# Performance work log

Measured on AMD Instinct MI355X. Metric: run time of the kernel, lower is better.

Reference implementation:

```python
import jax, jax.numpy as jnp
import numpy as np

N, E, H, NH, S, EF, K = 25000, 400000, 64, 4, 16, 8, 2
HS = H // NH  # head size


def _ln(x, w, b):
    m = x.mean(-1, keepdims=True)
    v = ((x - m) ** 2).mean(-1, keepdims=True)
    return (x - m) / jnp.sqrt(v + 1e-5) * w + b


def _seg_softmax(scores, seg, n):
    # scores: [E, NH], seg: [E] -> softmax over edges sharing the same dest node
    mx = jax.ops.segment_max(scores, seg, num_segments=n)
    e = jnp.exp(scores - mx[seg])
    s = jax.ops.segment_sum(e, seg, num_segments=n)
    return e / (s[seg] + 1e-9)


def _edge_layer(h, x_s, src, dest, ef, w1, w2, proj, gated):
    # h: [N,H] (already layer-normed). Gather, fused per-edge MLP (no bias).
    inp = jnp.concatenate([h[src], h[dest], x_s[src], x_s[dest], ef], axis=-1)  # [E,168]
    raw = jnp.maximum(inp @ w1.T, 0.0) @ w2.T  # [E,NH]
    if gated:
        w = jax.nn.sigmoid(raw)
    else:
        w = _seg_softmax(jax.nn.leaky_relu(raw) / jnp.sqrt(jnp.asarray(HS, raw.dtype)), dest, N)
    msg = h.reshape(N, NH, HS)[src] * w[:, :, None]          # [E,NH,HS]
    agg = jax.ops.segment_sum(msg, dest, num_segments=N)     # [N,NH,HS]
    return agg.reshape(N, H) @ proj.T, w


def _mlp(x, w1, b1, w2, b2):
    return jnp.maximum(x @ w1.T + b1, 0.0) @ w2.T + b2


def _forward(x, x_s, edge_features, fwd_w1, fwd_w2, fwd_proj, rev_w1, rev_w2, rev_proj,
             ln_w, ln_b, r_w1, r_b1, r_w2, r_b2, z_w1, z_b1, z_w2, z_b2,
             c_w1, c_b1, c_w2, c_b2, edge_index):
    src, dest = edge_index[0], edge_index[1]
    # forward-direction stacked attention hops
    h_fwd, fwd_ws = x, []
    for k in range(K):
        h_norm = _ln(h_fwd, ln_w, ln_b)
        msg, w = _edge_layer(h_norm, x_s, src, dest, edge_features,
                             fwd_w1[k], fwd_w2[k], fwd_proj[k], gated=False)
        h_fwd = h_fwd + msg
        fwd_ws.append(w)
    fwd_ws = jnp.stack(fwd_ws, axis=-1)  # [E,NH,K]
    # reverse-direction stacked gating hops (edge direction flipped)
    h_rev, rev_ws = x, []
    for k in range(K):
        h_norm = _ln(h_rev, ln_w, ln_b)
        msg, w = _edge_layer(h_norm, x_s, dest, src, edge_features,
                             rev_w1[k], rev_w2[k], rev_proj[k], gated=True)
        h_rev = h_rev + msg
        rev_ws.append(w)
    rev_ws = jnp.stack(rev_ws, axis=-1)  # [E,NH,K]
    messages = jnp.concatenate([h_fwd - x, h_rev - x], axis=-1)  # [N,2H]
    gate_input = jnp.concatenate([x, messages], axis=-1)          # [N,3H]
    r_gate = jax.nn.sigmoid(_mlp(gate_input, r_w1, r_b1, r_w2, r_b2))
    z_gate = jax.nn.sigmoid(_mlp(gate_input, z_w1, z_b1, z_w2, z_b2))
    cand_in = jnp.concatenate([r_gate * x, messages], axis=-1)
    cand = jnp.tanh(_mlp(cand_in, c_w1, c_b1, c_w2, c_b2))
    final_h = (1.0 - z_gate) * x + z_gate * cand
    return final_h, fwd_ws, rev_ws, z_gate, r_gate


def setup_inputs() -> dict:
    key = jax.random.key(0)
    ks = jax.random.split(key, 20)
    mlp_in = 2 * H + 2 * S + EF  # 168
    width = 2 * H                # 128
    gi, gw = 3 * H, 3 * H        # 192, 192

    def nrm(k, shape, fan_in):
        return jax.random.normal(k, shape, jnp.float32) / np.sqrt(fan_in)

    return {
        'x': jax.random.normal(ks[0], (N, H), jnp.float32),
        'x_s': jax.random.normal(ks[1], (N, S), jnp.float32),
        'edge_index': jax.random.randint(ks[2], (2, E), 0, N, jnp.int32),
        'edge_features': jax.random.normal(ks[3], (E, EF), jnp.float32),
        'fwd_w1': nrm(ks[4], (K, width, mlp_in), mlp_in),
        'fwd_w2': nrm(ks[5], (K, NH, width), width),
        'fwd_proj': nrm(ks[6], (K, H, H), H),
        'rev_w1': nrm(ks[7], (K, width, mlp_in), mlp_in),
        'rev_w2': nrm(ks[8], (K, NH, width), width),
        'rev_proj': nrm(ks[9], (K, H, H), H),
        'ln_w': jnp.ones((H,), jnp.float32),
        'ln_b': jnp.zeros((H,), jnp.float32),
        'r_w1': nrm(ks[10], (gw, gi), gi), 'r_b1': jnp.zeros((gw,), jnp.float32),
        'r_w2': nrm(ks[11], (H, gw), gw), 'r_b2': jnp.zeros((H,), jnp.float32),
        'z_w1': nrm(ks[12], (gw, gi), gi), 'z_b1': jnp.zeros((gw,), jnp.float32),
        'z_w2': nrm(ks[13], (H, gw), gw), 'z_b2': jnp.zeros((H,), jnp.float32),
        'c_w1': nrm(ks[14], (gw, gi), gi), 'c_b1': jnp.zeros((gw,), jnp.float32),
        'c_w2': nrm(ks[15], (H, gw), gw), 'c_b2': jnp.zeros((H,), jnp.float32),
    }


def reference(x, x_s, edge_index, edge_features, fwd_w1, fwd_w2, fwd_proj,
              rev_w1, rev_w2, rev_proj, ln_w, ln_b, r_w1, r_b1, r_w2, r_b2,
              z_w1, z_b1, z_w2, z_b2, c_w1, c_b1, c_w2, c_b2):
    return _forward(x, x_s, edge_features, fwd_w1, fwd_w2, fwd_proj,
                    rev_w1, rev_w2, rev_proj, ln_w, ln_b,
                    r_w1, r_b1, r_w2, r_b2, z_w1, z_b1, z_w2, z_b2,
                    c_w1, c_b1, c_w2, c_b2, edge_index)
```

## Files before the change

### kernel.cpp

```cpp
#include <hip/hip_runtime.h>
#include <hip/hip_fp16.h>
#include <math.h>

#define NN 25000
#define EE 400000
#define HH 64
#define NHEAD 4
#define SDIM 16
#define EFDIM 8
#define KHOP 2
#define MIN 168
#define WID 128
#define GIN 192
#define KP 96

typedef __attribute__((ext_vector_type(8))) short bf16x8;
typedef __attribute__((ext_vector_type(4))) float f32x4;
typedef unsigned short ushortT;
typedef unsigned int uintT;

__device__ __forceinline__ float wave_sum64(float v) {
#pragma unroll
  for (int m = 1; m <= 32; m <<= 1) v += __shfl_xor(v, m, 64);
  return v;
}

__device__ __forceinline__ ushortT f2b(float f) {
  uintT u = __float_as_uint(f);
  return (ushortT)((u + 0x7FFFu + ((u >> 16) & 1u)) >> 16);
}
__device__ __forceinline__ float b2f(ushortT h) {
  return __uint_as_float(((uintT)h) << 16);
}

union U4H8 {
  uint4 u;
  __half2 h[4];
};

__device__ __forceinline__ __half2 relu2(__half2 v) {
  union { __half2 h; uintT u; } x;
  x.h = v;
  uintT mask = ((x.u & 0x80008000u) >> 15) * 0xFFFFu;
  x.u &= ~mask;
  return x.h;
}

__global__ void k_histo2(const int* __restrict__ src, const int* __restrict__ dst,
                         int* __restrict__ cnt_s, int* __restrict__ cnt_d) {
  int e = blockIdx.x * 256 + threadIdx.x;
  if (e < EE) {
    atomicAdd(&cnt_d[dst[e]], 1);
    atomicAdd(&cnt_s[src[e]], 1);
  }
}

__global__ void k_scan2(const int* __restrict__ cnt_d, const int* __restrict__ cnt_s,
                        int* __restrict__ rp_d, int* __restrict__ rp_s) {
  const int* cnt = blockIdx.x ? cnt_s : cnt_d;
  int* rp = blockIdx.x ? rp_s : rp_d;
  __shared__ int part[1024];
  int t = threadIdx.x;
  const int CH = (NN + 1023) / 1024;
  int base = t * CH;
  int s = 0;
  for (int i = 0; i < CH; ++i) {
    int j = base + i;
    if (j < NN) s += cnt[j];
  }
  part[t] = s;
  __syncthreads();
  for (int off = 1; off < 1024; off <<= 1) {
    int v = (t >= off) ? part[t - off] : 0;
    __syncthreads();
    part[t] += v;
    __syncthreads();
  }
  int run = (t == 0) ? 0 : part[t - 1];
  for (int i = 0; i < CH; ++i) {
    int j = base + i;
    if (j < NN) { rp[j] = run; run += cnt[j]; }
  }
  if (t == 1023) rp[NN] = run;
}

__global__ void k_scatter2(const int* __restrict__ src, const int* __restrict__ dst,
                           const int* __restrict__ rp_s, const int* __restrict__ rp_d,
                           int* __restrict__ cur_s, int* __restrict__ cur_d,
                           int* __restrict__ eid_s, int* __restrict__ eid_d) {
  int e = blockIdx.x * 256 + threadIdx.x;
  if (e < EE) {
    int nd = dst[e];
    int pd = atomicAdd(&cur_d[nd], 1);
    eid_d[rp_d[nd] + pd] = e;
    int ns = src[e];
    int ps = atomicAdd(&cur_s[ns], 1);
    eid_s[rp_s[ns] + ps] = e;
  }
}

__global__ __launch_bounds__(256) void k_sortseg2(const int* __restrict__ rp_d,
                                                  const int* __restrict__ rp_s,
                                                  int* __restrict__ eid_d,
                                                  int* __restrict__ eid_s) {
  int gw = blockIdx.x * 4 + (threadIdx.x >> 6);
  int lane = threadIdx.x & 63;
  if (gw >= 2 * NN) return;
  const int* rp = (gw < NN) ? rp_d : rp_s;
  int* eids = (gw < NN) ? eid_d : eid_s;
  int node = (gw < NN) ? gw : gw - NN;
  int beg = rp[node], end = rp[node + 1];
  int deg = end - beg;
  if (deg <= 1) return;
  if (deg <= 64) {
    int v = (lane < deg) ? eids[beg + lane] : 0x7fffffff;
#pragma unroll
    for (int k = 2; k <= 64; k <<= 1) {
#pragma unroll
      for (int j = k >> 1; j > 0; j >>= 1) {
        int other = __shfl_xor(v, j, 64);
        bool takeMin = (((lane & k) == 0) == ((lane & j) == 0));
        v = takeMin ? min(v, other) : max(v, other);
      }
    }
    if (lane < deg) eids[beg + lane] = v;
  } else if (lane == 0) {
    for (int i = beg + 1; i < end; ++i) {
      int v = eids[i];
      int j = i - 1;
      while (j >= beg && eids[j] > v) { eids[j + 1] = eids[j]; --j; }
      eids[j + 1] = v;
    }
  }
}

__global__ void k_mkpos2(const int* __restrict__ eid_d, const int* __restrict__ eid_s,
                         const int* __restrict__ src, const int* __restrict__ dst,
                         const float* __restrict__ ef, int4* __restrict__ pos_f,
                         int4* __restrict__ pos_r, uint4* __restrict__ efh_f,
                         uint4* __restrict__ efh_r) {
  int i = blockIdx.x * 256 + threadIdx.x;
  if (i >= EE) return;
  int e1 = eid_d[i];
  pos_f[i] = make_int4(e1, src[e1], dst[e1], 0);
  int e2 = eid_s[i];
  pos_r[i] = make_int4(e2, dst[e2], src[e2], 0);
  {
    float4 a0 = *(const float4*)(ef + (size_t)e1 * EFDIM);
    float4 a1 = *(const float4*)(ef + (size_t)e1 * EFDIM + 4);
    U4H8 u;
    u.h[0] = __floats2half2_rn(a0.x, a0.y);
    u.h[1] = __floats2half2_rn(a0.z, a0.w);
    u.h[2] = __floats2half2_rn(a1.x, a1.y);
    u.h[3] = __floats2half2_rn(a1.z, a1.w);
    efh_f[i] = u.u;
  }
  {
    float4 b0 = *(const float4*)(ef + (size_t)e2 * EFDIM);
    float4 b1 = *(const float4*)(ef + (size_t)e2 * EFDIM + 4);
    U4H8 u;
    u.h[0] = __floats2half2_rn(b0.x, b0.y);
    u.h[1] = __floats2half2_rn(b0.z, b0.w);
    u.h[2] = __floats2half2_rn(b1.x, b1.y);
    u.h[3] = __floats2half2_rn(b1.z, b1.w);
    efh_r[i] = u.u;
  }
}

#define PACKN (256 * KP + 512 + 256)
__global__ void k_pack_bf(const float* __restrict__ fw1, const float* __restrict__ rw1,
                          const float* __restrict__ fw2, const float* __restrict__ rw2,
                          ushortT* __restrict__ pAB_all, __half2* __restrict__ w1e2_all,
                          __half2* __restrict__ w22_all) {
  int y = blockIdx.y;
  const float* w1 = (y < 2) ? fw1 + (size_t)y * WID * MIN
                            : rw1 + (size_t)(y - 2) * WID * MIN;
  const float* w2 = (y < 2) ? fw2 + (size_t)y * NHEAD * WID
                            : rw2 + (size_t)(y - 2) * NHEAD * WID;
  int i = blockIdx.x * 256 + threadIdx.x;
  if (i < 256 * KP) {
    int j = i / KP, k = i % KP;
    float v = 0.f;
    if (k < 80) {
      int row = (j < 128) ? j : j - 128;
      int col = (j < 128) ? (k < 64 ? k : k + 64) : (k < 64 ? k + 64 : k + 80);
      v = w1[row * MIN + col];
    }
    pAB_all[(size_t)y * 256 * KP + i] = f2b(v);
  } else if (i < 256 * KP + 512) {
    int jj = i - 256 * KP;
    int f = jj >> 6, jp = jj & 63;
    w1e2_all[y * 512 + jj] =
        __floats2half2_rn(w1[(2 * jp) * MIN + 160 + f], w1[(2 * jp + 1) * MIN + 160 + f]);
  } else if (i < PACKN) {
    int jj = i - 256 * KP - 512;
    int o = jj >> 6, jp = jj & 63;
    w22_all[y * 256 + jj] = __floats2half2_rn(w2[o * WID + 2 * jp], w2[o * WID + 2 * jp + 1]);
  }
}

#define CW1 (GIN * GIN)
#define CW2 (HH * GIN)
__global__ void k_cvt6(const float* __restrict__ r_w1, const float* __restrict__ z_w1,
                       const float* __restrict__ c_w1, const float* __restrict__ r_w2,
                       const float* __restrict__ z_w2, const float* __restrict__ c_w2,
                       ushortT* __restrict__ rzw1, ushortT* __restrict__ cw1,
                       ushortT* __restrict__ rw2, ushortT* __restrict__ zw2,
                       ushortT* __restrict__ cw2) {
  int i = blockIdx.x * 256 + threadIdx.x;
  if (i < CW1) rzw1[i] = f2b(r_w1[i]);
  else if (i < 2 * CW1) rzw1[i] = f2b(z_w1[i - CW1]);
  else if (i < 3 * CW1) cw1[i - 2 * CW1] = f2b(c_w1[i - 2 * CW1]);
  else if (i < 3 * CW1 + CW2) rw2[i - 3 * CW1] = f2b(r_w2[i - 3 * CW1]);
  else if (i < 3 * CW1 + 2 * CW2) zw2[i - 3 * CW1 - CW2] = f2b(z_w2[i - 3 * CW1 - CW2]);
  else if (i < 3 * CW1 + 3 * CW2) cw2[i - 3 * CW1 - 2 * CW2] = f2b(c_w2[i - 3 * CW1 - 2 * CW2]);
}

__global__ __launch_bounds__(256) void k_ln_init(
    const float* __restrict__ x, const float* __restrict__ xs,
    const float* __restrict__ lw, const float* __restrict__ lb,
    ushortT* __restrict__ ncf0, ushortT* __restrict__ ncr0,
    ushortT* __restrict__ ncf1, ushortT* __restrict__ ncr1) {
  int t = threadIdx.x;
  int node = blockIdx.x * 4 + (t >> 6), lane = t & 63;
  if (node >= NN) return;
  float v = x[(size_t)node * HH + lane];
  float mean = wave_sum64(v) * (1.0f / 64.0f);
  float d = v - mean;
  float var = wave_sum64(d * d) * (1.0f / 64.0f);
  ushortT val = f2b(d * rsqrtf(var + 1e-5f) * lw[lane] + lb[lane]);
  ncf0[(size_t)node * KP + lane] = val;
  ncr0[(size_t)node * KP + lane] = val;
  if (lane < SDIM) {
    ushortT xv = f2b(xs[(size_t)node * SDIM + lane]);
    ncf0[(size_t)node * KP + HH + lane] = xv;
    ncr0[(size_t)node * KP + HH + lane] = xv;
    ncf1[(size_t)node * KP + HH + lane] = xv;
    ncr1[(size_t)node * KP + HH + lane] = xv;
    ncf0[(size_t)node * KP + 80 + lane] = 0;
    ncr0[(size_t)node * KP + 80 + lane] = 0;
    ncf1[(size_t)node * KP + 80 + lane] = 0;
    ncr1[(size_t)node * KP + 80 + lane] = 0;
  }
}

__global__ __launch_bounds__(256) void k_proj2(
    const ushortT* __restrict__ Af, const ushortT* __restrict__ Ar,
    const ushortT* __restrict__ Wf, const ushortT* __restrict__ Wr,
    ushortT* __restrict__ Cf, ushortT* __restrict__ Cr) {
  const ushortT* A = blockIdx.y ? Ar : Af;
  const ushortT* W = blockIdx.y ? Wr : Wf;
  ushortT* C = blockIdx.y ? Cr : Cf;
  int w = threadIdx.x >> 6, l = threadIdx.x & 63;
  int m0 = blockIdx.x * 64 + w * 16;
  int rowa = m0 + (l & 15);
  int kb = l >> 4;
  bf16x8 afr0 = {0,0,0,0,0,0,0,0}, afr1 = afr0, afr2 = afr0;
  if (rowa < NN) {
    const ushortT* ap = A + (size_t)rowa * KP + kb * 8;
    afr0 = *(const bf16x8*)(ap);
    afr1 = *(const bf16x8*)(ap + 32);
    afr2 = *(const bf16x8*)(ap + 64);
  }
  int crow = m0 + (l >> 4) * 4;
  int ccol0 = l & 15;
  for (int n0 = 0; n0 < 256; n0 += 64) {
    f32x4 acc[4];
#pragma unroll
    for (int n = 0; n < 4; ++n) acc[n] = (f32x4){0.f, 0.f, 0.f, 0.f};
    const ushortT* wbase = W + (size_t)(n0 + (l & 15)) * KP + kb * 8;
#pragma unroll
    for (int n = 0; n < 4; ++n) {
      const ushortT* wp = wbase + (size_t)(16 * n) * KP;
      acc[n] = __builtin_amdgcn_mfma_f32_16x16x32_bf16(afr0, *(const bf16x8*)(wp), acc[n], 0, 0, 0);
      acc[n] = __builtin_amdgcn_mfma_f32_16x16x32_bf16(afr1, *(const bf16x8*)(wp + 32), acc[n], 0, 0, 0);
      acc[n] = __builtin_amdgcn_mfma_f32_16x16x32_bf16(afr2, *(const bf16x8*)(wp + 64), acc[n], 0, 0, 0);
    }
#pragma unroll
    for (int n = 0; n < 4; ++n) {
      int col = n0 + ccol0 + n * 16;
#pragma unroll
      for (int r = 0; r < 4; ++r) {
        int row = crow + r;
        if (row < NN)
          C[(size_t)row * 256 + col] = __half_as_ushort(__float2half(acc[n][r]));
      }
    }
  }
}

template <int ACT, int BF16OUT, int KD>
__global__ __launch_bounds__(256) void k_gemm2(
    const ushortT* __restrict__ A, int lda, const ushortT* __restrict__ W,
    const float* __restrict__ bias, void* __restrict__ Cout, int ldc, int M, int Nc,
    const float* __restrict__ zv, const float* __restrict__ xp) {
  constexpr int KS = KD / 32;
  int w = threadIdx.x >> 6, l = threadIdx.x & 63;
  int m0 = blockIdx.x * 64 + w * 16;
  int rowa = m0 + (l & 15);
  int kb = l >> 4;
  bf16x8 afr[KS];
#pragma unroll
  for (int ks = 0; ks < KS; ++ks) {
    afr[ks] = (bf16x8){0, 0, 0, 0, 0, 0, 0, 0};
    if (rowa < M) afr[ks] = *(const bf16x8*)(A + (size_t)rowa * lda + ks * 32 + kb * 8);
  }
  int crow = m0 + (l >> 4) * 4;
  int ccol0 = l & 15;
  for (int n0 = 0; n0 < Nc; n0 += 64) {
    f32x4 acc[4];
#pragma unroll
    for (int n = 0; n < 4; ++n) acc[n] = (f32x4){0.f, 0.f, 0.f, 0.f};
    const ushortT* wbase = W + (size_t)(n0 + (l & 15)) * KD + kb * 8;
#pragma unroll
    for (int n = 0; n < 4; ++n) {
      const ushortT* wp = wbase + (size_t)(16 * n) * KD;
#pragma unroll
      for (int ks = 0; ks < KS; ++ks)
        acc[n] = __builtin_amdgcn_mfma_f32_16x16x32_bf16(afr[ks], *(const bf16x8*)(wp + ks * 32),
                                                         acc[n], 0, 0, 0);
    }
#pragma unroll
    for (int n = 0; n < 4; ++n) {
      int col = n0 + ccol0 + n * 16;
      float bv = bias ? bias[col] : 0.f;
#pragma unroll
      for (int r = 0; r < 4; ++r) {
        int row = crow + r;
        if (row < M) {
          float v = acc[n][r] + bv;
          if (ACT == 1) v = fmaxf(v, 0.f);
          else if (ACT == 2) v = 1.f / (1.f + expf(-v));
          else if (ACT == 3) v = tanhf(v);
          else if (ACT == 5) {
            float z = zv[(size_t)row * HH + col];
            float xv = xp[(size_t)row * HH + col];
            v = (1.f - z) * xv + z * tanhf(v);
          }
          if (BF16OUT)
            ((ushortT*)Cout)[(size_t)row * ldc + col] = f2b(v);
          else
            ((float*)Cout)[(size_t)row * ldc + col] = v;
        }
      }
    }
  }
}

__global__ __launch_bounds__(256) void k_gemm_rz(
    const ushortT* __restrict__ hid, const ushortT* __restrict__ rw2,
    const ushortT* __restrict__ zw2, const float* __restrict__ rb2,
    const float* __restrict__ zb2, float* __restrict__ outR, float* __restrict__ outZ,
    const float* __restrict__ x, ushortT* __restrict__ gi) {
  int y = blockIdx.y;
  const ushortT* A = hid + (y ? GIN : 0);
  const ushortT* W = y ? zw2 : rw2;
  const float* bias = y ? zb2 : rb2;
  float* C = y ? outZ : outR;
  constexpr int KS = GIN / 32;
  int w = threadIdx.x >> 6, l = threadIdx.x & 63;
  int m0 = blockIdx.x * 64 + w * 16;
  int rowa = m0 + (l & 15);
  int kb = l >> 4;
  bf16x8 afr[KS];
#pragma unroll
  for (int ks = 0; ks < KS; ++ks) {
    afr[ks] = (bf16x8){0, 0, 0, 0, 0, 0, 0, 0};
    if (rowa < NN) afr[ks] = *(const bf16x8*)(A + (size_t)rowa * 384 + ks * 32 + kb * 8);
  }
  int crow = m0 + (l >> 4) * 4;
  int ccol0 = l & 15;
  f32x4 acc[4];
#pragma unroll
  for (int n = 0; n < 4; ++n) acc[n] = (f32x4){0.f, 0.f, 0.f, 0.f};
  const ushortT* wbase = W + (size_t)(l & 15) * GIN + kb * 8;
#pragma unroll
  for (int n = 0; n < 4; ++n) {
    const ushortT* wp = wbase + (size_t)(16 * n) * GIN;
#pragma unroll
    for (int ks = 0; ks < KS; ++ks)
      acc[n] = __builtin_amdgcn_mfma_f32_16x16x32_bf16(afr[ks], *(const bf16x8*)(wp + ks * 32),
                                                       acc[n], 0, 0, 0);
  }
#pragma unroll
  for (int n = 0; n < 4; ++n) {
    int col = ccol0 + n * 16;
    float bv = bias[col];
#pragma unroll
    for (int r = 0; r < 4; ++r) {
      int row = crow + r;
      if (row < NN) {
        float v = acc[n][r] + bv;
        float sig = 1.f / (1.f + expf(-v));
        C[(size_t)row * HH + col] = sig;
        if (y == 0)
          gi[(size_t)row * GIN + col] = f2b(sig * x[(size_t)row * HH + col]);
      }
    }
  }
}

__global__ __launch_bounds__(256) void k_edge3(
    const ushortT* __restrict__ cABf, const ushortT* __restrict__ cABr,
    const int4* __restrict__ pos_f, const int4* __restrict__ pos_r,
    const uint4* __restrict__ efh_f, const uint4* __restrict__ efh_r,
    const __half2* __restrict__ w1e2_f, const __half2* __restrict__ w1e2_r,
    const __half2* __restrict__ w22_f, const __half2* __restrict__ w22_r,
    float* __restrict__ s_seq, float* __restrict__ outRW,
    float* __restrict__ ws_seq, int hop) {
  int y = blockIdx.y;
  const __half2* cAB2 = (const __half2*)(y ? cABr : cABf);
  const int4* pos = y ? pos_r : pos_f;
  const uint4* efh = y ? efh_r : efh_f;
  const __half2* w1e2 = y ? w1e2_r : w1e2_f;
  const __half2* w22 = y ? w22_r : w22_f;
  __shared__ __half2 w1e2_s[8][64];
  __shared__ __half2 w22_s[4][64];
  int t = threadIdx.x;
  for (int i = t; i < 512; i += 256) w1e2_s[i >> 6][i & 63] = w1e2[i];
  if (t < 256) w22_s[t >> 6][t & 63] = w22[t];
  __syncthreads();
  int es = t >> 2, q = t & 3;
  size_t ii = (size_t)blockIdx.x * 64 + es;
  int4 pr = pos[ii];
  const __half2* cA2 = cAB2 + (size_t)pr.y * 128;
  const __half2* cB2 = cAB2 + (size_t)pr.z * 128 + 64;
  U4H8 efu;
  efu.u = efh[ii];
  __half2 efb[8];
#pragma unroll
  for (int f2v = 0; f2v < 4; ++f2v) {
    efb[2 * f2v] = __half2half2(__low2half(efu.h[f2v]));
    efb[2 * f2v + 1] = __half2half2(__high2half(efu.h[f2v]));
  }
  float pf[4] = {0.f, 0.f, 0.f, 0.f};
#pragma unroll
  for (int c = 0; c < 4; ++c) {
    int jp0 = c * 16 + q * 4;
    U4H8 ua, ub;
    ua.u = *(const uint4*)(cA2 + jp0);
    ub.u = *(const uint4*)(cB2 + jp0);
    __half2 h2v[4];
#pragma unroll
    for (int i2 = 0; i2 < 4; ++i2) h2v[i2] = __hadd2(ua.h[i2], ub.h[i2]);
#pragma unroll
    for (int f = 0; f < 8; ++f) {
      U4H8 wv;
      wv.u = *(const uint4*)(&w1e2_s[f][jp0]);
#pragma unroll
      for (int i2 = 0; i2 < 4; ++i2) h2v[i2] = __hfma2(efb[f], wv.h[i2], h2v[i2]);
    }
#pragma unroll
    for (int i2 = 0; i2 < 4; ++i2) h2v[i2] = relu2(h2v[i2]);
#pragma unroll
    for (int o = 0; o < 4; ++o) {
      U4H8 wv;
      wv.u = *(const uint4*)(&w22_s[o][jp0]);
      __half2 p2 = __hmul2(h2v[0], wv.h[0]);
      p2 = __hfma2(h2v[1], wv.h[1], p2);
      p2 = __hfma2(h2v[2], wv.h[2], p2);
      p2 = __hfma2(h2v[3], wv.h[3], p2);
      pf[o] += __low2float(p2) + __high2float(p2);
    }
  }
#pragma unroll
  for (int m = 1; m <= 2; m <<= 1) {
    pf[0] += __shfl_xor(pf[0], m, 64);
    pf[1] += __shfl_xor(pf[1], m, 64);
    pf[2] += __shfl_xor(pf[2], m, 64);
    pf[3] += __shfl_xor(pf[3], m, 64);
  }
  float pv = (q == 0) ? pf[0] : (q == 1) ? pf[1] : (q == 2) ? pf[2] : pf[3];
  if (y) {
    float sig = 1.f / (1.f + expf(-pv));
    outRW[(size_t)pr.x * (NHEAD * KHOP) + q * KHOP + hop] = sig;
    ws_seq[ii * 4 + q] = sig;
  } else {
    s_seq[ii * 4 + q] = (pv > 0.f ? pv : 0.01f * pv) * 0.25f;
  }
}

template <int DO_LN, int DO_GATE>
__global__ __launch_bounds__(256) void k_softagg3(
    const ushortT* __restrict__ ncf, const ushortT* __restrict__ ncr,
    ushortT* __restrict__ ncf_n, ushortT* __restrict__ ncr_n,
    const float* __restrict__ s_seq, const float* __restrict__ ws_seq, int hop,
    const int* __restrict__ rp_d, const int* __restrict__ rp_s,
    const int4* __restrict__ pos_f, const int4* __restrict__ pos_r,
    const float* __restrict__ proj_f, const float* __restrict__ proj_r,
    float* __restrict__ h_f, float* __restrict__ h_r, float* __restrict__ wout,
    const float* __restrict__ lnw, const float* __restrict__ lnb,
    const float* __restrict__ x, ushortT* __restrict__ gi) {
  int y = blockIdx.y;
  const ushortT* hn_bf = y ? ncr : ncf;
  const int* rp = y ? rp_s : rp_d;
  const int4* pos = y ? pos_r : pos_f;
  const float* proj = y ? proj_r : proj_f;
  float* h = y ? h_r : h_f;
  __shared__ float proj_s[64][68];
  __shared__ float agg_s[4][64];
  __shared__ float w_s[4][64][4];
  int t = threadIdx.x;
  for (int i = t; i < 4096; i += 256) proj_s[i >> 6][i & 63] = proj[i];
  int wvi = t >> 6, lane = t & 63;
  int node = blockIdx.x * 4 + wvi;
  __syncthreads();

  float acc = 0.f;
  int beg = 0, end = 0;
  if (node < NN) {
    beg = rp[node];
    end = rp[node + 1];
    int deg = end - beg;
    float mxv = 0.f, invv = 0.f;
    if (y == 0 && deg > 0) {
      int li = lane >> 2, o = lane & 3;
      if (deg <= 64) {
        int i0 = beg + li;
        int ee4[4];
        float sv[4];
#pragma unroll
        for (int u = 0; u < 4; ++u) {
          int idx = i0 + u * 16;
          bool val = idx < end;
          int id2 = val ? idx : beg;
          ee4[u] = pos[id2].x;
          float v = s_seq[(size_t)id2 * 4 + o];
          sv[u] = val ? v : -1e30f;
        }
        float mx = fmaxf(fmaxf(sv[0], sv[1]), fmaxf(sv[2], sv[3]));
#pragma unroll
        for (int m = 4; m <= 32; m <<= 1) mx = fmaxf(mx, __shfl_xor(mx, m, 64));
        float ex[4];
        float sum = 0.f;
#pragma unroll
        for (int u = 0; u < 4; ++u) {
          ex[u] = (sv[u] > -1e29f) ? expf(sv[u] - mx) : 0.f;
          sum += ex[u];
        }
#pragma unroll
        for (int m = 4; m <= 32; m <<= 1) sum += __shfl_xor(sum, m, 64);
        float inv = 1.f / (sum + 1e-9f);
#pragma unroll
        for (int u = 0; u < 4; ++u) {
          if (i0 + u * 16 < end) {
            float wv = ex[u] * inv;
            wout[(size_t)ee4[u] * (NHEAD * KHOP) + o * KHOP + hop] = wv;
            w_s[wvi][li + u * 16][o] = wv;
          }
        }
      } else {
        float mx = -1e30f;
        for (int ii = beg + li; ii < end; ii += 16)
          mx = fmaxf(mx, s_seq[(size_t)ii * 4 + o]);
#pragma unroll
        for (int m = 4; m <= 32; m <<= 1) mx = fmaxf(mx, __shfl_xor(mx, m, 64));
        float sum = 0.f;
        for (int ii = beg + li; ii < end; ii += 16)
          sum += expf(s_seq[(size_t)ii * 4 + o] - mx);
#pragma unroll
        for (int m = 4; m <= 32; m <<= 1) sum += __shfl_xor(sum, m, 64);
        float inv = 1.f / (sum + 1e-9f);
        for (int ii = beg + li; ii < end; ii += 16) {
          wout[(size_t)pos[ii].x * (NHEAD * KHOP) + o * KHOP + hop] =
              expf(s_seq[(size_t)ii * 4 + o] - mx) * inv;
        }
        mxv = mx;
        invv = inv;
      }
    }
    int hd = lane >> 4;
    float mx_hd = 0.f, inv_hd = 0.f;
    if (y == 0) {
      mx_hd = __shfl(mxv, hd, 64);
      inv_hd = __shfl(invv, hd, 64);
    }
    bool useLds = ((end - beg) <= 64);
    for (int ii = beg; ii < end; ii += 8) {
      int idxv[8];
      int other[8];
      float wv8[8];
      float hv[8];
#pragma unroll
      for (int u = 0; u < 8; ++u) {
        int idx = ii + u;
        idxv[u] = (idx < end) ? idx : beg;
      }
#pragma unroll
      for (int u = 0; u < 8; ++u) other[u] = pos[idxv[u]].y;
#pragma unroll
      for (int u = 0; u < 8; ++u) {
        if (y == 0) {
          if (useLds)
            wv8[u] = w_s[wvi][idxv[u] - beg][hd];
          else
            wv8[u] = expf(s_seq[(size_t)idxv[u] * 4 + hd] - mx_hd) * inv_hd;
        } else {
          wv8[u] = ws_seq[(size_t)idxv[u] * 4 + hd];
        }
      }
#pragma unroll
      for (int u = 0; u < 8; ++u)
        hv[u] = b2f(hn_bf[(size_t)other[u] * KP + lane]);
#pragma unroll
      for (int u = 0; u < 8; ++u) {
        float w = (ii + u < end) ? wv8[u] : 0.f;
        acc += w * hv[u];
      }
    }
  }
  agg_s[wvi][lane] = acc;
  __syncthreads();
  if (node < NN) {
    float m = 0.f;
#pragma unroll
    for (int hh = 0; hh < 64; hh += 4) {
      float4 p = *(const float4*)(&proj_s[lane][hh]);
      m += p.x * agg_s[wvi][hh] + p.y * agg_s[wvi][hh + 1] +
           p.z * agg_s[wvi][hh + 2] + p.w * agg_s[wvi][hh + 3];
    }
    size_t g = (size_t)node * HH + lane;
    float hnew = h[g] + m;
    h[g] = hnew;
    if (DO_LN) {
      float mean = wave_sum64(hnew) * (1.0f / 64.0f);
      float d = hnew - mean;
      float var = wave_sum64(d * d) * (1.0f / 64.0f);
      ushortT val = f2b(d * rsqrtf(var + 1e-5f) * lnw[lane] + lnb[lane]);
      (y ? ncr_n : ncf_n)[(size_t)node * KP + lane] = val;
    }
    if (DO_GATE) {
      float xv = x[g];
      if (y == 0) {
        gi[(size_t)node * GIN + lane] = f2b(xv);
        gi[(size_t)node * GIN + 64 + lane] = f2b(hnew - xv);
      } else {
        gi[(size_t)node * GIN + 128 + lane] = f2b(hnew - xv);
      }
    }
  }
}

extern "C" void kernel_launch(void* const* d_in, const int* in_sizes, int n_in,
                              void* d_out, int out_size, void* d_ws, size_t ws_size,
                              hipStream_t stream) {
  const float* x = (const float*)d_in[0];
  const float* xs = (const float*)d_in[1];
  const int* ei = (const int*)d_in[2];
  const float* ef = (const float*)d_in[3];
  const float* fw1 = (const float*)d_in[4];
  const float* fw2 = (const float*)d_in[5];
  const float* fpj = (const float*)d_in[6];
  const float* rw1 = (const float*)d_in[7];
  const float* rw2 = (const float*)d_in[8];
  const float* rpj = (const float*)d_in[9];
  const float* lnw = (const float*)d_in[10];
  const float* lnb = (const float*)d_in[11];
  const float* r_w1 = (const float*)d_in[12];
  const float* r_b1 = (const float*)d_in[13];
  const float* r_w2 = (const float*)d_in[14];
  const float* r_b2 = (const float*)d_in[15];
  const float* z_w1 = (const float*)d_in[16];
  const float* z_b1 = (const float*)d_in[17];
  const float* z_w2 = (const float*)d_in[18];
  const float* z_b2 = (const float*)d_in[19];
  const float* c_w1 = (const float*)d_in[20];
  const float* c_b1 = (const float*)d_in[21];
  const float* c_w2 = (const float*)d_in[22];
  const float* c_b2 = (const float*)d_in[23];
  const int* srcp = ei;
  const int* dstp = ei + EE;

  float* outF = (float*)d_out;
  float* outFW = outF + (size_t)NN * HH;
  float* outRW = outFW + (size_t)EE * NHEAD * KHOP;
  float* outZ = outRW + (size_t)EE * NHEAD * KHOP;
  float* outR = outZ + (size_t)NN * HH;

  char* Wb = (char*)d_ws;
  size_t off = 0;
  auto alloc = [&](size_t bytes) -> void* {
    void* p = Wb + off;
    off += (bytes + 255) & ~(size_t)255;
    return p;
  };
  float* h_fwd = (float*)alloc((size_t)NN * HH * 4);
  float* h_rev = (float*)alloc((size_t)NN * HH * 4);
  ushortT* ncat_f0 = (ushortT*)alloc((size_t)NN * KP * 2);
  ushortT* ncat_r0 = (ushortT*)alloc((size_t)NN * KP * 2);
  ushortT* ncat_f1 = (ushortT*)alloc((size_t)NN * KP * 2);
  ushortT* ncat_r1 = (ushortT*)alloc((size_t)NN * KP * 2);
  float* s_seq = (float*)alloc((size_t)EE * NHEAD * 4);
  float* ws_seq = (float*)alloc((size_t)EE * NHEAD * 4);
  char* big = (char*)alloc((size_t)2 * NN * 256 * 2);
  ushortT* cAB_f = (ushortT*)big;
  ushortT* cAB_r = (ushortT*)(big + (size_t)NN * 256 * 2);
  ushortT* hid_bf = (ushortT*)big;
  ushortT* gi_bf = (ushortT*)alloc((size_t)NN * GIN * 2);
  ushortT* packAB_bf = (ushortT*)alloc((size_t)4 * 256 * KP * 2);
  __half2* w1e2h = (__half2*)alloc((size_t)4 * 512 * 4);
  __half2* w22h = (__half2*)alloc((size_t)4 * 256 * 4);
  ushortT* rzw1_bf = (ushortT*)alloc((size_t)384 * GIN * 2);
  ushortT* rw2_bf = (ushortT*)alloc((size_t)HH * GIN * 2);
  ushortT* zw2_bf = (ushortT*)alloc((size_t)HH * GIN * 2);
  ushortT* cw1_bf = (ushortT*)alloc((size_t)GIN * GIN * 2);
  ushortT* cw2_bf = (ushortT*)alloc((size_t)HH * GIN * 2);
  float* rz_b1 = (float*)alloc(384 * 4);
  int* rp_d = (int*)alloc((NN + 8) * 4);
  int* rp_s = (int*)alloc((NN + 8) * 4);
  int* cur2 = (int*)alloc((size_t)2 * NN * 4);
  int* cur_d = cur2;
  int* cur_s = cur2 + NN;
  int* eid_d = (int*)alloc((size_t)EE * 4);
  int* eid_s = (int*)alloc((size_t)EE * 4);
  int4* pos_f = (int4*)alloc((size_t)EE * 16);
  int4* pos_r = (int4*)alloc((size_t)EE * 16);
  uint4* efh_f = (uint4*)alloc((size_t)EE * 16);
  uint4* efh_r = (uint4*)alloc((size_t)EE * 16);

  (void)hipMemcpyAsync(h_fwd, x, (size_t)NN * HH * 4, hipMemcpyDeviceToDevice, stream);
  (void)hipMemcpyAsync(h_rev, x, (size_t)NN * HH * 4, hipMemcpyDeviceToDevice, stream);
  (void)hipMemcpyAsync(rz_b1, r_b1, GIN * 4, hipMemcpyDeviceToDevice, stream);
  (void)hipMemcpyAsync(rz_b1 + GIN, z_b1, GIN * 4, hipMemcpyDeviceToDevice, stream);

  const int EB = (EE + 255) / 256, NW = (NN + 3) / 4;
  const int PB = (PACKN + 255) / 256;

  dim3 gPack(PB, 4);
  k_pack_bf<<<gPack, 256, 0, stream>>>(fw1, rw1, fw2, rw2, packAB_bf, w1e2h, w22h);
  k_cvt6<<<(3 * CW1 + 3 * CW2 + 255) / 256, 256, 0, stream>>>(
      r_w1, z_w1, c_w1, r_w2, z_w2, c_w2, rzw1_bf, cw1_bf, rw2_bf, zw2_bf, cw2_bf);

  (void)hipMemsetAsync(cur2, 0, (size_t)2 * NN * 4, stream);
  k_histo2<<<EB, 256, 0, stream>>>(srcp, dstp, cur_s, cur_d);
  k_scan2<<<2, 1024, 0, stream>>>(cur_d, cur_s, rp_d, rp_s);
  (void)hipMemsetAsync(cur2, 0, (size_t)2 * NN * 4, stream);
  k_scatter2<<<EB, 256, 0, stream>>>(srcp, dstp, rp_s, rp_d, cur_s, cur_d, eid_s, eid_d);
  k_sortseg2<<<(2 * NN + 3) / 4, 256, 0, stream>>>(rp_d, rp_s, eid_d, eid_s);
  k_mkpos2<<<EB, 256, 0, stream>>>(eid_d, eid_s, srcp, dstp, ef, pos_f, pos_r, efh_f, efh_r);

  k_ln_init<<<NW, 256, 0, stream>>>(x, xs, lnw, lnb, ncat_f0, ncat_r0, ncat_f1, ncat_r1);

  const int MB64 = (NN + 63) / 64;
  dim3 gProj(MB64, 2), gEdge(EE / 64, 2), gAgg(NW, 2);
  for (int k = 0; k < KHOP; ++k) {
    const ushortT* nf = k ? ncat_f1 : ncat_f0;
    const ushortT* nr = k ? ncat_r1 : ncat_r0;
    k_proj2<<<gProj, 256, 0, stream>>>(nf, nr,
                                       packAB_bf + (size_t)k * 256 * KP,
                                       packAB_bf + (size_t)(2 + k) * 256 * KP,
                                       cAB_f, cAB_r);
    k_edge3<<<gEdge, 256, 0, stream>>>(cAB_f, cAB_r, pos_f, pos_r, efh_f, efh_r,
                                       w1e2h + (size_t)k * 512,
                                       w1e2h + (size_t)(2 + k) * 512,
                                       w22h + (size_t)k * 256,
                                       w22h + (size_t)(2 + k) * 256,
                                       s_seq, outRW, ws_seq, k);
    if (k == 0)
      k_softagg3<1, 0><<<gAgg, 256, 0, stream>>>(
          nf, nr, ncat_f1, ncat_r1, s_seq, ws_seq, k, rp_d, rp_s, pos_f, pos_r,
          fpj + (size_t)k * HH * HH, rpj + (size_t)k * HH * HH, h_fwd, h_rev, outFW,
          lnw, lnb, x, gi_bf);
    else
      k_softagg3<0, 1><<<gAgg, 256, 0, stream>>>(
          nf, nr, ncat_f1, ncat_r1, s_seq, ws_seq, k, rp_d, rp_s, pos_f, pos_r,
          fpj + (size_t)k * HH * HH, rpj + (size_t)k * HH * HH, h_fwd, h_rev, outFW,
          lnw, lnb, x, gi_bf);
  }

  k_gemm2<1, 1, GIN><<<MB64, 256, 0, stream>>>(gi_bf, GIN, rzw1_bf, rz_b1, hid_bf,
                                               384, NN, 384, nullptr, nullptr);
  dim3 gRZ(MB64, 2);
  k_gemm_rz<<<gRZ, 256, 0, stream>>>(hid_bf, rw2_bf, zw2_bf, r_b2, z_b2, outR, outZ,
                                     x, gi_bf);
  k_gemm2<1, 1, GIN><<<MB64, 256, 0, stream>>>(gi_bf, GIN, cw1_bf, c_b1, hid_bf, GIN,
                                               NN, GIN, nullptr, nullptr);
  k_gemm2<5, 0, GIN><<<MB64, 256, 0, stream>>>(hid_bf, GIN, cw2_bf, c_b2, outF, HH,
                                               NN, HH, outZ, x);
}
```

Baseline: 547.0 us.

## Process four nodes per wave in softagg and stage neighbor offsets in LDS

The aggregation kernel now loops over four destination nodes per wave, so each block handles 16 nodes and the 16 KB projection matrix load is amortized over four times more nodes. For small-degree nodes, both directions stage neighbor row offsets and edge weights in LDS once, with a lane subset doing the loads, so the gather loop only reads LDS indices instead of re-reading pos from global memory. The per-node block-wide syncthreads is removed, but the LDS agg buffer is written and read within a wave without a barrier, and the grid is four times smaller, which lowers parallelism.

```diff
diff --git a/kernel.cpp b/kernel.cpp
--- a/kernel.cpp
+++ b/kernel.cpp
@@ -481,7 +481,7 @@
 }
 
 template <int DO_LN, int DO_GATE>
-__global__ __launch_bounds__(256) void k_softagg3(
+__global__ __launch_bounds__(256) void k_softagg4(
     const ushortT* __restrict__ ncf, const ushortT* __restrict__ ncr,
     ushortT* __restrict__ ncf_n, ushortT* __restrict__ ncr_n,
     const float* __restrict__ s_seq, const float* __restrict__ ws_seq, int hop,
@@ -500,32 +500,33 @@
   __shared__ float proj_s[64][68];
   __shared__ float agg_s[4][64];
   __shared__ float w_s[4][64][4];
+  __shared__ int ot_s[4][64];
   int t = threadIdx.x;
   for (int i = t; i < 4096; i += 256) proj_s[i >> 6][i & 63] = proj[i];
   int wvi = t >> 6, lane = t & 63;
-  int node = blockIdx.x * 4 + wvi;
   __syncthreads();
 
-  float acc = 0.f;
-  int beg = 0, end = 0;
-  if (node < NN) {
-    beg = rp[node];
-    end = rp[node + 1];
+  for (int it = 0; it < 4; ++it) {
+    int node = blockIdx.x * 16 + wvi * 4 + it;
+    if (node >= NN) continue;
+    int beg = rp[node], end = rp[node + 1];
     int deg = end - beg;
+    bool small = (deg <= 64);
     float mxv = 0.f, invv = 0.f;
-    if (y == 0 && deg > 0) {
-      int li = lane >> 2, o = lane & 3;
-      if (deg <= 64) {
-        int i0 = beg + li;
+    int li = lane >> 2, o = lane & 3;
+    if (deg > 0 && small) {
+      int i0 = beg + li;
+      if (y == 0) {
         int ee4[4];
         float sv[4];
 #pragma unroll
         for (int u = 0; u < 4; ++u) {
           int idx = i0 + u * 16;
           bool val = idx < end;
-          int id2 = val ? idx : beg;
-          ee4[u] = pos[id2].x;
-          float v = s_seq[(size_t)id2 * 4 + o];
+          int4 pr = pos[val ? idx : beg];
+          ee4[u] = pr.x;
+          if (o == 0 && val) ot_s[wvi][li + u * 16] = pr.y * KP;
+          float v = s_seq[(size_t)(val ? idx : beg) * 4 + o];
           sv[u] = val ? v : -1e30f;
         }
         float mx = fmaxf(fmaxf(sv[0], sv[1]), fmaxf(sv[2], sv[3]));
@@ -550,6 +551,21 @@
           }
         }
       } else {
+#pragma unroll
+        for (int u = 0; u < 4; ++u) {
+          int idx = i0 + u * 16;
+          bool val = idx < end;
+          if (val) {
+            if (o == 0) {
+              int4 pr = pos[idx];
+              ot_s[wvi][li + u * 16] = pr.y * KP;
+            }
+            w_s[wvi][li + u * 16][o] = ws_seq[(size_t)idx * 4 + o];
+          }
+        }
+      }
+    } else if (deg > 0) {
+      if (y == 0) {
         float mx = -1e30f;
         for (int ii = beg + li; ii < end; ii += 16)
           mx = fmaxf(mx, s_seq[(size_t)ii * 4 + o]);
@@ -570,48 +586,36 @@
       }
     }
     int hd = lane >> 4;
-    float mx_hd = 0.f, inv_hd = 0.f;
-    if (y == 0) {
-      mx_hd = __shfl(mxv, hd, 64);
-      inv_hd = __shfl(invv, hd, 64);
-    }
-    bool useLds = ((end - beg) <= 64);
-    for (int ii = beg; ii < end; ii += 8) {
-      int idxv[8];
-      int other[8];
-      float wv8[8];
-      float hv[8];
-#pragma unroll
-      for (int u = 0; u < 8; ++u) {
-        int idx = ii + u;
-        idxv[u] = (idx < end) ? idx : beg;
-      }
-#pragma unroll
-      for (int u = 0; u < 8; ++u) other[u] = pos[idxv[u]].y;
-#pragma unroll
-      for (int u = 0; u < 8; ++u) {
-        if (y == 0) {
-          if (useLds)
-            wv8[u] = w_s[wvi][idxv[u] - beg][hd];
-          else
-            wv8[u] = expf(s_seq[(size_t)idxv[u] * 4 + hd] - mx_hd) * inv_hd;
-        } else {
-          wv8[u] = ws_seq[(size_t)idxv[u] * 4 + hd];
+    float acc = 0.f;
+    if (small) {
+      for (int ii = 0; ii < deg; ii += 8) {
+#pragma unroll
+        for (int u = 0; u < 8; ++u) {
+          int ed = ii + u;
+          int edc = (ed < deg) ? ed : 0;
+          int ot = ot_s[wvi][edc];
+          float w = w_s[wvi][edc][hd];
+          float hv = b2f(hn_bf[(size_t)ot + lane]);
+          acc += ((ed < deg) ? w : 0.f) * hv;
         }
       }
-#pragma unroll
-      for (int u = 0; u < 8; ++u)
-        hv[u] = b2f(hn_bf[(size_t)other[u] * KP + lane]);
-#pragma unroll
-      for (int u = 0; u < 8; ++u) {
-        float w = (ii + u < end) ? wv8[u] : 0.f;
-        acc += w * hv[u];
-      }
-    }
-  }
-  agg_s[wvi][lane] = acc;
-  __syncthreads();
-  if (node < NN) {
+    } else {
+      float mx_hd = 0.f, inv_hd = 0.f;
+      if (y == 0) {
+        mx_hd = __shfl(mxv, hd, 64);
+        inv_hd = __shfl(invv, hd, 64);
+      }
+      for (int ii = beg; ii < end; ++ii) {
+        int4 pr = pos[ii];
+        float w;
+        if (y == 0)
+          w = expf(s_seq[(size_t)ii * 4 + hd] - mx_hd) * inv_hd;
+        else
+          w = ws_seq[(size_t)ii * 4 + hd];
+        acc += w * b2f(hn_bf[(size_t)pr.y * KP + lane]);
+      }
+    }
+    agg_s[wvi][lane] = acc;
     float m = 0.f;
 #pragma unroll
     for (int hh = 0; hh < 64; hh += 4) {
@@ -742,7 +746,8 @@
   k_ln_init<<<NW, 256, 0, stream>>>(x, xs, lnw, lnb, ncat_f0, ncat_r0, ncat_f1, ncat_r1);
 
   const int MB64 = (NN + 63) / 64;
-  dim3 gProj(MB64, 2), gEdge(EE / 64, 2), gAgg(NW, 2);
+  const int NB16 = (NN + 15) / 16;
+  dim3 gProj(MB64, 2), gEdge(EE / 64, 2), gAgg(NB16, 2);
   for (int k = 0; k < KHOP; ++k) {
     const ushortT* nf = k ? ncat_f1 : ncat_f0;
     const ushortT* nr = k ? ncat_r1 : ncat_r0;
@@ -757,12 +762,12 @@
                                        w22h + (size_t)(2 + k) * 256,
                                        s_seq, outRW, ws_seq, k);
     if (k == 0)
-      k_softagg3<1, 0><<<gAgg, 256, 0, stream>>>(
+      k_softagg4<1, 0><<<gAgg, 256, 0, stream>>>(
           nf, nr, ncat_f1, ncat_r1, s_seq, ws_seq, k, rp_d, rp_s, pos_f, pos_r,
           fpj + (size_t)k * HH * HH, rpj + (size_t)k * HH * HH, h_fwd, h_rev, outFW,
           lnw, lnb, x, gi_bf);
     else
-      k_softagg3<0, 1><<<gAgg, 256, 0, stream>>>(
+      k_softagg4<0, 1><<<gAgg, 256, 0, stream>>>(
           nf, nr, ncat_f1, ncat_r1, s_seq, ws_seq, k, rp_d, rp_s, pos_f, pos_r,
           fpj + (size_t)k * HH * HH, rpj + (size_t)k * HH * HH, h_fwd, h_rev, outFW,
           lnw, lnb, x, gi_bf);
```

Result: faster. 533.9 us (-2.4%).
